# Kernel tuning notes

Measured on AMD Instinct MI355X. Metric: run time of the kernel, lower is better.

The kernel has to match this reference:

```python
import jax, jax.numpy as jnp
import numpy as np

B, F, C, H, W = 256, 16, 256, 32, 32

def setup_inputs() -> dict:
    key = jax.random.key(0)
    kx, kk = jax.random.split(key)
    x = jax.random.normal(kx, (B, C, H, W), dtype=jnp.float32)
    # kaiming_normal init: std = sqrt(2 / fan_in), fan_in = C*H*W
    std = float(np.sqrt(2.0 / (C * H * W)))
    kernel = jax.random.normal(kk, (F, C, H, W), dtype=jnp.float32) * std
    return {"x": x, "kernel": kernel}

def reference(x, kernel):
    # (x[:,None] * kernel[None]).sum((-1,-2)) == einsum over spatial dims, per channel
    y = jnp.einsum('bchw,fchw->bfc', x, kernel)  # [B, F, C]
    return y.reshape(y.shape[0], -1)  # [B, F*C]
```

## Files before the change

kernel.cpp:

```cpp
#include <hip/hip_runtime.h>
#include <hip/hip_bf16.h>


constexpr int Bb = 256;
constexpr int Ff = 16;
constexpr int Cc = 256;
constexpr int HW = 1024;
constexpr int CHW = Cc * HW;

constexpr int BT = 128;
constexpr int RB = 4;
constexpr int NTHREADS = (BT / RB) * 16;
constexpr int NJ = HW / 4 / 16;

__device__ __forceinline__ float dot4(float4 a, float4 b) {
    return a.x * b.x + a.y * b.y + a.z * b.z + a.w * b.w;
}
__device__ __forceinline__ float red16(float v) {
    v += __shfl_xor(v, 1);
    v += __shfl_xor(v, 2);
    v += __shfl_xor(v, 4);
    v += __shfl_xor(v, 8);
    return v;
}

template <bool TO_WS>
__global__ __launch_bounds__(NTHREADS)
void sle_kernel(const float* __restrict__ x, const float* __restrict__ k,
                float* __restrict__ dst) {
    __shared__ float ldsK[Ff * HW];

    const int t   = threadIdx.x;
    const int thw = t & 15;
    const int tbg = t >> 4;

    const int g     = blockIdx.x;
    const int c     = (g & 7) * 32 + ((g >> 3) & 31);
    const int btile = g >> 8;
    const int b0    = btile * BT + tbg * RB;

    {
        const int fr = t >> 5, lane32 = t & 31;
        const float4* src = (const float4*)(k + (size_t)fr * CHW + (size_t)c * HW);
        float4* dstk = (float4*)(ldsK + fr * HW);
#pragma unroll
        for (int q = 0; q < 8; ++q)
            dstk[lane32 + 32 * q] = src[lane32 + 32 * q];
    }
    __syncthreads();

    const float* xb = x + (size_t)c * HW;
    const int xo0 = (b0 + 0) * CHW;
    const int xo1 = (b0 + 1) * CHW;
    const int xo2 = (b0 + 2) * CHW;
    const int xo3 = (b0 + 3) * CHW;

    float4 a00={0,0,0,0}, a01={0,0,0,0}, a02={0,0,0,0}, a03={0,0,0,0};
    float4 a10={0,0,0,0}, a11={0,0,0,0}, a12={0,0,0,0}, a13={0,0,0,0};
    float4 a20={0,0,0,0}, a21={0,0,0,0}, a22={0,0,0,0}, a23={0,0,0,0};
    float4 a30={0,0,0,0}, a31={0,0,0,0}, a32={0,0,0,0}, a33={0,0,0,0};

#pragma unroll 2
    for (int j = 0; j < NJ; ++j) {
        const int off = 4 * (thw + 16 * j);
        const float4 xv0 = *(const float4*)(xb + xo0 + off);
        const float4 xv1 = *(const float4*)(xb + xo1 + off);
        const float4 xv2 = *(const float4*)(xb + xo2 + off);
        const float4 xv3 = *(const float4*)(xb + xo3 + off);

#define ACC_G(G, A0, A1, A2, A3) {                                      \
        const float* kp = ldsK + (4 * (G)) * HW + off;                  \
        const float4 k0 = *(const float4*)(kp);                         \
        const float4 k1 = *(const float4*)(kp + HW);                    \
        const float4 k2 = *(const float4*)(kp + 2 * HW);                \
        const float4 k3 = *(const float4*)(kp + 3 * HW);                \
        A0.x += dot4(xv0, k0); A0.y += dot4(xv0, k1);                   \
        A0.z += dot4(xv0, k2); A0.w += dot4(xv0, k3);                   \
        A1.x += dot4(xv1, k0); A1.y += dot4(xv1, k1);                   \
        A1.z += dot4(xv1, k2); A1.w += dot4(xv1, k3);                   \
        A2.x += dot4(xv2, k0); A2.y += dot4(xv2, k1);                   \
        A2.z += dot4(xv2, k2); A2.w += dot4(xv2, k3);                   \
        A3.x += dot4(xv3, k0); A3.y += dot4(xv3, k1);                   \
        A3.z += dot4(xv3, k2); A3.w += dot4(xv3, k3); }

        ACC_G(0, a00, a10, a20, a30)
        ACC_G(1, a01, a11, a21, a31)
        ACC_G(2, a02, a12, a22, a32)
        ACC_G(3, a03, a13, a23, a33)
#undef ACC_G
    }

#define RED4(A) { A.x = red16(A.x); A.y = red16(A.y); \
                  A.z = red16(A.z); A.w = red16(A.w); }
    RED4(a00) RED4(a01) RED4(a02) RED4(a03)
    RED4(a10) RED4(a11) RED4(a12) RED4(a13)
    RED4(a20) RED4(a21) RED4(a22) RED4(a23)
    RED4(a30) RED4(a31) RED4(a32) RED4(a33)
#undef RED4

    __syncthreads();
    if (thw == 0) {
        float4* r0 = (float4*)(ldsK + (tbg * RB + 0) * Ff);
        float4* r1 = (float4*)(ldsK + (tbg * RB + 1) * Ff);
        float4* r2 = (float4*)(ldsK + (tbg * RB + 2) * Ff);
        float4* r3 = (float4*)(ldsK + (tbg * RB + 3) * Ff);
        r0[0] = a00; r0[1] = a01; r0[2] = a02; r0[3] = a03;
        r1[0] = a10; r1[1] = a11; r1[2] = a12; r1[3] = a13;
        r2[0] = a20; r2[1] = a21; r2[2] = a22; r2[3] = a23;
        r3[0] = a30; r3[1] = a31; r3[2] = a32; r3[3] = a33;
    }
    __syncthreads();

    if (TO_WS) {
        float4 v = *(const float4*)(ldsK + 4 * t);
        *(float4*)(dst + (size_t)c * (Bb * Ff) + btile * (BT * Ff) + 4 * t) = v;
    } else {
#pragma unroll
        for (int i = 0; i < (BT * Ff) / NTHREADS; ++i) {
            const int idx = t + NTHREADS * i;
            const int bl  = idx >> 4;
            const int f   = idx & 15;
            dst[(size_t)(btile * BT + bl) * (Ff * Cc) + f * Cc + c] = ldsK[idx];
        }
    }
}

constexpr int TS = 64;
__global__ __launch_bounds__(256)
void trans_kernel(const float* __restrict__ yT, float* __restrict__ out) {
    __shared__ float tl[TS][TS + 1];
    const int t  = threadIdx.x;
    const int bi = blockIdx.x & 63;
    const int bj = blockIdx.x >> 6;
    const int r0 = bi * TS, c0 = bj * TS;
    const int rr = t & 15, cl = t >> 4;

#pragma unroll
    for (int q = 0; q < 4; ++q) {
        const int c_local = cl + 16 * q;
        const float4 v = *(const float4*)(yT + (size_t)(c0 + c_local) * 4096
                                              + r0 + 4 * rr);
        tl[c_local][4 * rr + 0] = v.x;
        tl[c_local][4 * rr + 1] = v.y;
        tl[c_local][4 * rr + 2] = v.z;
        tl[c_local][4 * rr + 3] = v.w;
    }
    __syncthreads();
#pragma unroll
    for (int q = 0; q < 4; ++q) {
        const int r_local = cl + 16 * q;
        float4 v;
        v.x = tl[4 * rr + 0][r_local];
        v.y = tl[4 * rr + 1][r_local];
        v.z = tl[4 * rr + 2][r_local];
        v.w = tl[4 * rr + 3][r_local];
        *(float4*)(out + (size_t)(r0 + r_local) * 256 + c0 + 4 * rr) = v;
    }
}

extern "C" void kernel_launch(void* const* d_in, const int* in_sizes, int n_in,
                              void* d_out, int out_size, void* d_ws, size_t ws_size,
                              hipStream_t stream) {
    const float* x = (const float*)d_in[0];
    const float* k = (const float*)d_in[1];
    float* out = (float*)d_out;
    const int grid = Cc * (Bb / BT);
    const size_t need = (size_t)Cc * Bb * Ff * sizeof(float);
    if (ws_size >= need && d_ws != nullptr) {
        float* yT = (float*)d_ws;
        sle_kernel<true><<<grid, NTHREADS, 0, stream>>>(x, k, yT);
        trans_kernel<<<256, 256, 0, stream>>>(yT, out);
    } else {
        sle_kernel<false><<<grid, NTHREADS, 0, stream>>>(x, k, out);
    }
}
```

Baseline: 391.5 us.

## Process two channels per block with 64-batch tiles and 512 threads

```diff
diff --git a/kernel.cpp b/kernel.cpp
--- a/kernel.cpp
+++ b/kernel.cpp
@@ -8,9 +8,9 @@
 constexpr int HW = 1024;
 constexpr int CHW = Cc * HW;
 
-constexpr int BT = 128;
+constexpr int BT = 64;
 constexpr int RB = 4;
-constexpr int NTHREADS = (BT / RB) * 16;
+constexpr int NTHREADS = 512;
 constexpr int NJ = HW / 4 / 16;
 
 __device__ __forceinline__ float dot4(float4 a, float4 b) {
@@ -28,32 +28,38 @@
 __global__ __launch_bounds__(NTHREADS)
 void sle_kernel(const float* __restrict__ x, const float* __restrict__ k,
                 float* __restrict__ dst) {
-    __shared__ float ldsK[Ff * HW];
+    __shared__ float ldsK[2 * Ff * HW];
 
     const int t   = threadIdx.x;
     const int thw = t & 15;
     const int tbg = t >> 4;
+    const int csel = tbg & 1;
+    const int bg   = tbg >> 1;
 
     const int g     = blockIdx.x;
-    const int c     = (g & 7) * 32 + ((g >> 3) & 31);
-    const int btile = g >> 8;
-    const int b0    = btile * BT + tbg * RB;
+    const int cp    = g & 127;
+    const int btile = g >> 7;
+    const int c0    = 2 * cp;
+    const int b0    = btile * BT + bg * RB;
 
     {
-        const int fr = t >> 5, lane32 = t & 31;
-        const float4* src = (const float4*)(k + (size_t)fr * CHW + (size_t)c * HW);
-        float4* dstk = (float4*)(ldsK + fr * HW);
+        const int r = t >> 4, lane16 = t & 15;
+        const int f = r & 15, cs = r >> 4;
+        const float4* src = (const float4*)(k + (size_t)f * CHW
+                                              + (size_t)(c0 + cs) * HW);
+        float4* dstk = (float4*)(ldsK + (size_t)cs * (Ff * HW) + f * HW);
 #pragma unroll
-        for (int q = 0; q < 8; ++q)
-            dstk[lane32 + 32 * q] = src[lane32 + 32 * q];
+        for (int q = 0; q < 16; ++q)
+            dstk[lane16 + 16 * q] = src[lane16 + 16 * q];
     }
     __syncthreads();
 
-    const float* xb = x + (size_t)c * HW;
+    const float* xb = x + (size_t)(c0 + csel) * HW;
     const int xo0 = (b0 + 0) * CHW;
     const int xo1 = (b0 + 1) * CHW;
     const int xo2 = (b0 + 2) * CHW;
     const int xo3 = (b0 + 3) * CHW;
+    const float* kbase = ldsK + (size_t)csel * (Ff * HW);
 
     float4 a00={0,0,0,0}, a01={0,0,0,0}, a02={0,0,0,0}, a03={0,0,0,0};
     float4 a10={0,0,0,0}, a11={0,0,0,0}, a12={0,0,0,0}, a13={0,0,0,0};
@@ -69,7 +75,7 @@
         const float4 xv3 = *(const float4*)(xb + xo3 + off);
 
 #define ACC_G(G, A0, A1, A2, A3) {                                      \
-        const float* kp = ldsK + (4 * (G)) * HW + off;                  \
+        const float* kp = kbase + (4 * (G)) * HW + off;                 \
         const float4 k0 = *(const float4*)(kp);                         \
         const float4 k1 = *(const float4*)(kp + HW);                    \
         const float4 k2 = *(const float4*)(kp + 2 * HW);                \
@@ -100,10 +106,11 @@
 
     __syncthreads();
     if (thw == 0) {
-        float4* r0 = (float4*)(ldsK + (tbg * RB + 0) * Ff);
-        float4* r1 = (float4*)(ldsK + (tbg * RB + 1) * Ff);
-        float4* r2 = (float4*)(ldsK + (tbg * RB + 2) * Ff);
-        float4* r3 = (float4*)(ldsK + (tbg * RB + 3) * Ff);
+        const int base = csel * (BT * Ff) + (bg * RB) * Ff;
+        float4* r0 = (float4*)(ldsK + base + 0 * Ff);
+        float4* r1 = (float4*)(ldsK + base + 1 * Ff);
+        float4* r2 = (float4*)(ldsK + base + 2 * Ff);
+        float4* r3 = (float4*)(ldsK + base + 3 * Ff);
         r0[0] = a00; r0[1] = a01; r0[2] = a02; r0[3] = a03;
         r1[0] = a10; r1[1] = a11; r1[2] = a12; r1[3] = a13;
         r2[0] = a20; r2[1] = a21; r2[2] = a22; r2[3] = a23;
@@ -112,15 +119,21 @@
     __syncthreads();
 
     if (TO_WS) {
-        float4 v = *(const float4*)(ldsK + 4 * t);
-        *(float4*)(dst + (size_t)c * (Bb * Ff) + btile * (BT * Ff) + 4 * t) = v;
+        const int e  = 4 * t;
+        const int cs = e >> 10;
+        const int rem = e & 1023;
+        float4 v = *(const float4*)(ldsK + e);
+        *(float4*)(dst + (size_t)(c0 + cs) * (Bb * Ff)
+                       + (size_t)btile * (BT * Ff) + rem) = v;
     } else {
 #pragma unroll
-        for (int i = 0; i < (BT * Ff) / NTHREADS; ++i) {
+        for (int i = 0; i < (2 * BT * Ff) / NTHREADS; ++i) {
             const int idx = t + NTHREADS * i;
-            const int bl  = idx >> 4;
+            const int cs  = idx >> 10;
+            const int bl  = (idx >> 4) & 63;
             const int f   = idx & 15;
-            dst[(size_t)(btile * BT + bl) * (Ff * Cc) + f * Cc + c] = ldsK[idx];
+            dst[(size_t)(btile * BT + bl) * (Ff * Cc) + f * Cc + (c0 + cs)]
+                = ldsK[idx];
         }
     }
 }
@@ -164,7 +177,7 @@
     const float* x = (const float*)d_in[0];
     const float* k = (const float*)d_in[1];
     float* out = (float*)d_out;
-    const int grid = Cc * (Bb / BT);
+    const int grid = (Cc / 2) * (Bb / BT);
     const size_t need = (size_t)Cc * Bb * Ff * sizeof(float);
     if (ws_size >= need && d_ws != nullptr) {
         float* yT = (float*)d_ws;
```

After: 394.2 us. About the same (+0.7%).
